# Kernel optimization log

Hardware: AMD Instinct MI355X
Metric: run time of the kernel (lower is better)

The kernel has to match this reference:

```python
import jax, jax.numpy as jnp
import numpy as np

B, N, K = 8, 4096, 16          # batch, points, kNN neighbors
IN_F, D, L, NUM_CLS = 3, 128, 2, 40  # in_features, hidden dim, transformer blocks, classes


def setup_inputs() -> dict:
    key = jax.random.key(0)
    ks = jax.random.split(key, 13)

    def w(k, shape):
        fan_in = shape[-2]
        return (jax.random.normal(k, shape, jnp.float32) / np.sqrt(fan_in).astype(np.float32))

    return {
        "features": jax.random.normal(ks[0], (B, N, IN_F), jnp.float32),
        "pos": jax.random.normal(ks[1], (B, N, 3), jnp.float32),
        "W_embed": w(ks[2], (IN_F, D)),
        "Wq": w(ks[3], (L, D, D)),
        "Wk": w(ks[4], (L, D, D)),
        "Wv": w(ks[5], (L, D, D)),
        "P1": w(ks[6], (L, 3, D)),   # position-encoding MLP layer 1
        "P2": w(ks[7], (L, D, D)),   # position-encoding MLP layer 2
        "G1": w(ks[8], (L, D, D)),   # attention (gamma) MLP layer 1
        "G2": w(ks[9], (L, D, D)),   # attention (gamma) MLP layer 2
        "Wo": w(ks[10], (L, D, D)),  # output projection per block
        "W_cls1": w(ks[11], (D, D)),
        "W_cls2": w(ks[12], (D, NUM_CLS)),
    }


def _gather(x, idx):
    # x: [B,N,C], idx: [B,N,K] -> [B,N,K,C]
    return jax.vmap(lambda xb, ib: xb[ib])(x, idx)


def _forward(features, pos, W_embed, Wq, Wk, Wv, P1, P2, G1, G2, Wo, W_cls1, W_cls2):
    # point-wise embedding MLP
    x = jax.nn.relu(features @ W_embed)  # [B,N,D]

    # kNN in euclidean space (indices, incl. self)
    sq = jnp.sum(pos * pos, axis=-1)                      # [B,N]
    d2 = sq[:, :, None] + sq[:, None, :] - 2.0 * jnp.einsum("bnc,bmc->bnm", pos, pos)
    _, idx = jax.lax.top_k(-d2, K)                        # [B,N,K]

    rel = pos[:, :, None, :] - _gather(pos, idx)          # [B,N,K,3]

    for l in range(L):
        q = x @ Wq[l]                                     # [B,N,D]
        k = x @ Wk[l]
        v = x @ Wv[l]
        kj = _gather(k, idx)                              # [B,N,K,D]
        vj = _gather(v, idx)
        # relative position encoding MLP
        delta = jax.nn.relu(rel @ P1[l]) @ P2[l]          # [B,N,K,D]
        # vector attention: gamma MLP over (q_i - k_j + delta)
        g = q[:, :, None, :] - kj + delta
        logits = jax.nn.relu(g @ G1[l]) @ G2[l]           # [B,N,K,D]
        attn = jax.nn.softmax(logits, axis=2)             # over K neighbors
        agg = jnp.sum(attn * (vj + delta), axis=2)        # [B,N,D]
        x = x + agg @ Wo[l]                               # residual

    pooled = jnp.max(x, axis=1)                           # [B,D] global max pool
    h = jax.nn.relu(pooled @ W_cls1)
    return h @ W_cls2                                     # [B,NUM_CLS]


def reference(features, pos, W_embed, Wq, Wk, Wv, P1, P2, G1, G2, Wo, W_cls1, W_cls2):
    return _forward(features, pos, W_embed, Wq, Wk, Wv, P1, P2, G1, G2, Wo, W_cls1, W_cls2)
```

## Files before the change

### kernel.cpp

```cpp
#include <hip/hip_runtime.h>
#include <hip/hip_bf16.h>
#include <float.h>

#define BB 8
#define NN 4096
#define KNN 16
#define Dh 128
#define NPTS (BB*NN)
#define NPART 4
#define PARTSZ (NN/NPART)

typedef __attribute__((ext_vector_type(8))) short bf16x8;
typedef __attribute__((ext_vector_type(8))) unsigned short u16x8;
typedef __attribute__((ext_vector_type(4))) float f32x4;

#define MFMA16(a,b,c) __builtin_amdgcn_mfma_f32_16x16x32_bf16(a,b,c,0,0,0)

__device__ __forceinline__ unsigned short f2b(float f) {
  __hip_bfloat16 h = __float2bfloat16(f);
  return *(unsigned short*)&h;
}
__device__ __forceinline__ unsigned pack_bf2(float lo, float hi) {
  __hip_bfloat16 l = __float2bfloat16(lo), h = __float2bfloat16(hi);
  return (unsigned)(*(unsigned short*)&l) | ((unsigned)(*(unsigned short*)&h) << 16);
}
__device__ __forceinline__ float b2f(unsigned short s) {
  union { unsigned u; float f; } v; v.u = ((unsigned)s) << 16; return v.f;
}
__device__ __forceinline__ float blo(unsigned u) {
  union { unsigned u; float f; } v; v.u = u << 16; return v.f;
}
__device__ __forceinline__ float bhi(unsigned u) {
  union { unsigned u; float f; } v; v.u = u & 0xffff0000u; return v.f;
}
__device__ __forceinline__ int swz16(int row) { return (row >> 2) << 4; }

__global__ __launch_bounds__(256) void embed_kernel(
    const float* __restrict__ f, const float* __restrict__ We, float* __restrict__ x) {
  int i = blockIdx.x * 256 + threadIdx.x;
  if (i >= NPTS * Dh) return;
  int p = i >> 7, d = i & 127;
  float f0 = f[p*3+0], f1 = f[p*3+1], f2 = f[p*3+2];
  float v = f0 * We[0*Dh + d] + f1 * We[1*Dh + d] + f2 * We[2*Dh + d];
  x[i] = fmaxf(v, 0.f);
}

__global__ __launch_bounds__(256) void knn_part_kernel(
    const float* __restrict__ pos, float* __restrict__ pd2,
    unsigned short* __restrict__ pix) {
  __shared__ float4 cand[PARTSZ];
  int b = blockIdx.z, part = blockIdx.y;
  const float* pb = pos + (size_t)b * NN * 3;
  int c0 = part * PARTSZ;
  for (int i = threadIdx.x; i < PARTSZ; i += 256) {
    float X = pb[(c0+i)*3+0], Y = pb[(c0+i)*3+1], Z = pb[(c0+i)*3+2];
    cand[i] = make_float4(X, Y, Z, X*X + Y*Y + Z*Z);
  }
  __syncthreads();

  int q = blockIdx.x * 256 + threadIdx.x;
  float qx = pb[q*3+0], qy = pb[q*3+1], qz = pb[q*3+2];
  float qs = qx*qx + qy*qy + qz*qz;

  float val[KNN]; int ind[KNN];
  float cmax; int cslot;

  #pragma unroll
  for (int t = 0; t < KNN; t++) {
    float4 c = cand[t];
    val[t] = qs + c.w - 2.f*(qx*c.x + qy*c.y + qz*c.z);
    ind[t] = t;
  }
  cmax = val[0]; cslot = 0;
  #pragma unroll
  for (int i = 1; i < KNN; i++)
    if (val[i] >= cmax) { cmax = val[i]; cslot = i; }

  float bv0=0.f,bv1=0.f,bv2=0.f,bv3=0.f,bv4=0.f,bv5=0.f,bv6=0.f,bv7=0.f;
  int   bi0=0,  bi1=0,  bi2=0,  bi3=0,  bi4=0,  bi5=0,  bi6=0,  bi7=0;
  int   cnt = 0;

#define DRAIN_SLOT(S, BV, BI)                                      \
  { bool act = ((S) < cnt) && ((BV) < cmax);                       \
    if (__ballot(act)) {                                           \
      _Pragma("unroll")                                            \
      for (int i = 0; i < KNN; i++) {                              \
        bool r = act && (i == cslot);                              \
        val[i] = r ? (BV) : val[i];                                \
        ind[i] = r ? (BI) : ind[i];                                \
      }                                                            \
      cmax = val[0]; cslot = 0;                                    \
      _Pragma("unroll")                                            \
      for (int i = 1; i < KNN; i++)                                \
        if (val[i] >= cmax) { cmax = val[i]; cslot = i; }          \
    } }
#define DRAIN_ALL                                                  \
  { DRAIN_SLOT(0, bv0, bi0) DRAIN_SLOT(1, bv1, bi1)                \
    DRAIN_SLOT(2, bv2, bi2) DRAIN_SLOT(3, bv3, bi3)                \
    DRAIN_SLOT(4, bv4, bi4) DRAIN_SLOT(5, bv5, bi5)                \
    DRAIN_SLOT(6, bv6, bi6) DRAIN_SLOT(7, bv7, bi7) cnt = 0; }

  for (int m = KNN; m < PARTSZ; m++) {
    float4 c = cand[m];
    float d2 = qs + c.w - 2.f*(qx*c.x + qy*c.y + qz*c.z);
    if (d2 < cmax) {
      bv0 = (cnt == 0) ? d2 : bv0;  bi0 = (cnt == 0) ? m : bi0;
      bv1 = (cnt == 1) ? d2 : bv1;  bi1 = (cnt == 1) ? m : bi1;
      bv2 = (cnt == 2) ? d2 : bv2;  bi2 = (cnt == 2) ? m : bi2;
      bv3 = (cnt == 3) ? d2 : bv3;  bi3 = (cnt == 3) ? m : bi3;
      bv4 = (cnt == 4) ? d2 : bv4;  bi4 = (cnt == 4) ? m : bi4;
      bv5 = (cnt == 5) ? d2 : bv5;  bi5 = (cnt == 5) ? m : bi5;
      bv6 = (cnt == 6) ? d2 : bv6;  bi6 = (cnt == 6) ? m : bi6;
      bv7 = (cnt == 7) ? d2 : bv7;  bi7 = (cnt == 7) ? m : bi7;
      cnt++;
    }
    if (__ballot(cnt == 8)) DRAIN_ALL
  }
  if (__ballot(cnt > 0)) DRAIN_ALL

#undef DRAIN_SLOT
#undef DRAIN_ALL

  size_t base = ((size_t)(b*NN + q) * NPART + part) * KNN;
  #pragma unroll
  for (int i = 0; i < KNN; i++) {
    pd2[base + i] = val[i];
    pix[base + i] = (unsigned short)(b*NN + c0 + ind[i]);
  }
}

__global__ __launch_bounds__(256) void knn_merge_kernel(
    const float* __restrict__ pd2, const unsigned short* __restrict__ pix,
    unsigned short* __restrict__ idxout) {
  int p = blockIdx.x * 256 + threadIdx.x;
  size_t base = (size_t)p * NPART * KNN;

  float val[KNN]; int ind[KNN];
  #pragma unroll
  for (int i = 0; i < KNN; i++) { val[i] = FLT_MAX; ind[i] = 0; }
  float cmax = FLT_MAX; int cslot = 0;

  for (int t = 0; t < NPART*KNN; t++) {
    float d2 = pd2[base + t];
    int j = pix[base + t];
    if (d2 < cmax) {
      #pragma unroll
      for (int i = 0; i < KNN; i++) if (i == cslot) { val[i] = d2; ind[i] = j; }
      cmax = val[0]; cslot = 0;
      #pragma unroll
      for (int i = 1; i < KNN; i++) if (val[i] >= cmax) { cmax = val[i]; cslot = i; }
    }
  }
  #pragma unroll
  for (int i = 0; i < KNN; i++) idxout[(size_t)p*KNN + i] = (unsigned short)ind[i];
}

__global__ __launch_bounds__(256) void wprep_all_kernel(
    const float* __restrict__ W0, const float* __restrict__ W1,
    const float* __restrict__ W2, const float* __restrict__ W3,
    const float* __restrict__ W4, const float* __restrict__ W5,
    const float* __restrict__ W6, unsigned short* __restrict__ wT) {
  const float* srcs[7] = {W0, W1, W2, W3, W4, W5, W6};
  int z = blockIdx.z, m = blockIdx.y;
  const float* W = srcs[z] + m*16384;
  unsigned short* WT = wT + z*32768 + m*16384;
  int t = blockIdx.x * 256 + threadIdx.x;
  int o = t >> 7, i = t & 127;
  WT[o*128 + i] = f2b(W[i*128 + o]);
}

__global__ __launch_bounds__(256) void qkv_kernel(
    const float* __restrict__ x,
    const unsigned short* __restrict__ QT, const unsigned short* __restrict__ KT,
    const unsigned short* __restrict__ VT,
    unsigned short* __restrict__ qb, unsigned* __restrict__ kvb) {
  int w = threadIdx.x >> 6, l = threadIdx.x & 63;
  int lr = l & 15, lg = l >> 4;
  int R = blockIdx.x * 64 + w * 16;
  const float* xr = x + (size_t)(R + lr) * Dh + lg * 8;
  bf16x8 a[4];
  #pragma unroll
  for (int kt = 0; kt < 4; kt++) {
    bf16x8 av;
    #pragma unroll
    for (int j = 0; j < 8; j++) av[j] = (short)f2b(xr[kt*32 + j]);
    a[kt] = av;
  }
  #pragma unroll
  for (int n = 0; n < 8; n++) {
    f32x4 c = {0.f, 0.f, 0.f, 0.f};
    #pragma unroll
    for (int kt = 0; kt < 4; kt++)
      c = MFMA16(a[kt], *(const bf16x8*)&QT[(n*16 + lr)*Dh + kt*32 + lg*8], c);
    #pragma unroll
    for (int r = 0; r < 4; r++)
      qb[(size_t)(R + lg*4 + r)*Dh + n*16 + lr] = f2b(c[r]);
  }
  #pragma unroll
  for (int n = 0; n < 8; n++) {
    f32x4 ck = {0.f, 0.f, 0.f, 0.f}, cv = {0.f, 0.f, 0.f, 0.f};
    #pragma unroll
    for (int kt = 0; kt < 4; kt++) {
      ck = MFMA16(a[kt], *(const bf16x8*)&KT[(n*16 + lr)*Dh + kt*32 + lg*8], ck);
      cv = MFMA16(a[kt], *(const bf16x8*)&VT[(n*16 + lr)*Dh + kt*32 + lg*8], cv);
    }
    #pragma unroll
    for (int r = 0; r < 4; r++)
      kvb[(size_t)(R + lg*4 + r)*Dh + n*16 + lr] = pack_bf2(ck[r], cv[r]);
  }
}

struct PtCtx {
  int jA, jC[4];
  float rx, ry, rz;
  unsigned short qv[8];
};
__device__ __forceinline__ void load_ctx(PtCtx& c, int p,
    const unsigned short* __restrict__ idxb, const float* __restrict__ pos,
    const unsigned short* __restrict__ qb, int lr, int lg) {
  c.jA = idxb[(size_t)p*KNN + lr];
  #pragma unroll
  for (int r = 0; r < 4; r++) c.jC[r] = idxb[(size_t)p*KNN + lg*4 + r];
  float px0 = pos[p*3+0], py0 = pos[p*3+1], pz0 = pos[p*3+2];
  c.rx = px0 - pos[c.jA*3+0];
  c.ry = py0 - pos[c.jA*3+1];
  c.rz = pz0 - pos[c.jA*3+2];
  #pragma unroll
  for (int n = 0; n < 8; n++) c.qv[n] = qb[(size_t)p*Dh + n*16 + lr];
}

__global__ void __attribute__((amdgpu_flat_work_group_size(512, 512)))
__attribute__((amdgpu_waves_per_eu(2, 2)))
fused_mega_kernel(
    const unsigned short* __restrict__ qb, const unsigned* __restrict__ kvb,
    const unsigned short* __restrict__ idxb, const float* __restrict__ pos,
    const float* __restrict__ P1,
    const unsigned short* __restrict__ P2T, const unsigned short* __restrict__ G1T,
    const unsigned short* __restrict__ G2T, unsigned short* __restrict__ aggb) {
  __shared__ __align__(16) unsigned short wB[3][16384];
  __shared__ __align__(16) unsigned short trans[8][2048];
  int tid = threadIdx.x;
  int wv = tid >> 6, l = tid & 63;
  int lr = l & 15, lg = l >> 4;
  const int swz = (lr & 7) << 3;
  const int swtR = swz16(lr);

  int orig = (blockIdx.x & 7) * 32 + (blockIdx.x >> 3);

  {
    const unsigned short* srcs[3] = {P2T, G1T, G2T};
    #pragma unroll
    for (int z = 0; z < 3; z++) {
      const unsigned short* src = srcs[z];
      for (int t = tid * 8; t < 16384; t += 512 * 8) {
        int dst = t ^ (((t >> 7) & 7) << 3);
        *(u16x8*)&wB[z][dst] = *(const u16x8*)&src[t];
      }
    }
  }
  __syncthreads();

  unsigned short* tb = trans[wv];
  int p0 = orig * 128 + wv * 16;

  PtCtx cur, nxt;
  load_ctx(cur, p0, idxb, pos, qb, lr, lg);
  nxt = cur;

  #pragma unroll 1
  for (int i = 0; i < 16; i++) {
    int p = p0 + i;

    const unsigned* kvp0 = kvb + (size_t)cur.jC[0]*Dh;
    const unsigned* kvp1 = kvb + (size_t)cur.jC[1]*Dh;
    const unsigned* kvp2 = kvb + (size_t)cur.jC[2]*Dh;
    const unsigned* kvp3 = kvb + (size_t)cur.jC[3]*Dh;
    unsigned kvr[8][4];
    #pragma unroll
    for (int n = 0; n < 8; n++) {
      kvr[n][0] = kvp0[n*16 + lr];
      kvr[n][1] = kvp1[n*16 + lr];
      kvr[n][2] = kvp2[n*16 + lr];
      kvr[n][3] = kvp3[n*16 + lr];
    }

    bf16x8 aT[4];
    #pragma unroll
    for (int kt = 0; kt < 4; kt++) {
      int c0 = kt*32 + lg*8;
      float4 pa0 = *(const float4*)&P1[c0],        pa1 = *(const float4*)&P1[c0+4];
      float4 pb0 = *(const float4*)&P1[Dh+c0],     pb1 = *(const float4*)&P1[Dh+c0+4];
      float4 pc0 = *(const float4*)&P1[2*Dh+c0],   pc1 = *(const float4*)&P1[2*Dh+c0+4];
      bf16x8 av;
      av[0] = (short)f2b(fmaxf(cur.rx*pa0.x + cur.ry*pb0.x + cur.rz*pc0.x, 0.f));
      av[1] = (short)f2b(fmaxf(cur.rx*pa0.y + cur.ry*pb0.y + cur.rz*pc0.y, 0.f));
      av[2] = (short)f2b(fmaxf(cur.rx*pa0.z + cur.ry*pb0.z + cur.rz*pc0.z, 0.f));
      av[3] = (short)f2b(fmaxf(cur.rx*pa0.w + cur.ry*pb0.w + cur.rz*pc0.w, 0.f));
      av[4] = (short)f2b(fmaxf(cur.rx*pa1.x + cur.ry*pb1.x + cur.rz*pc1.x, 0.f));
      av[5] = (short)f2b(fmaxf(cur.rx*pa1.y + cur.ry*pb1.y + cur.rz*pc1.y, 0.f));
      av[6] = (short)f2b(fmaxf(cur.rx*pa1.z + cur.ry*pb1.z + cur.rz*pc1.z, 0.f));
      av[7] = (short)f2b(fmaxf(cur.rx*pa1.w + cur.ry*pb1.w + cur.rz*pc1.w, 0.f));
      aT[kt] = av;
    }

    f32x4 dlt[8];
    #pragma unroll
    for (int n = 0; n < 8; n++) {
      f32x4 c = {0.f, 0.f, 0.f, 0.f};
      #pragma unroll
      for (int kt = 0; kt < 4; kt++)
        c = MFMA16(aT[kt], *(const bf16x8*)&wB[0][((n*16 + lr)*Dh + kt*32 + lg*8) ^ swz], c);
      dlt[n] = c;
    }

    #pragma unroll
    for (int n = 0; n < 8; n++) {
      float q = b2f(cur.qv[n]);
      #pragma unroll
      for (int r = 0; r < 4; r++) {
        unsigned kv = kvr[n][r];
        int row = lg*4 + r, ch = n*16 + lr;
        tb[(row*Dh + ch) ^ swz16(row)] = f2b(q - blo(kv) + dlt[n][r]);
        dlt[n][r] += bhi(kv);
      }
    }

    if (i < 15) load_ctx(nxt, p + 1, idxb, pos, qb, lr, lg);

    bf16x8 ag[4];
    #pragma unroll
    for (int kt = 0; kt < 4; kt++)
      ag[kt] = *(const bf16x8*)&tb[(lr*Dh + kt*32 + lg*8) ^ swtR];
    f32x4 hh[8];
    #pragma unroll
    for (int n = 0; n < 8; n++) {
      f32x4 c = {0.f, 0.f, 0.f, 0.f};
      #pragma unroll
      for (int kt = 0; kt < 4; kt++)
        c = MFMA16(ag[kt], *(const bf16x8*)&wB[1][((n*16 + lr)*Dh + kt*32 + lg*8) ^ swz], c);
      hh[n] = c;
    }
    #pragma unroll
    for (int n = 0; n < 8; n++) {
      #pragma unroll
      for (int r = 0; r < 4; r++) {
        int row = lg*4 + r, ch = n*16 + lr;
        tb[(row*Dh + ch) ^ swz16(row)] = f2b(fmaxf(hh[n][r], 0.f));
      }
    }

    bf16x8 ah[4];
    #pragma unroll
    for (int kt = 0; kt < 4; kt++)
      ah[kt] = *(const bf16x8*)&tb[(lr*Dh + kt*32 + lg*8) ^ swtR];
    f32x4 lgt[8];
    #pragma unroll
    for (int n = 0; n < 8; n++) {
      f32x4 c = {0.f, 0.f, 0.f, 0.f};
      #pragma unroll
      for (int kt = 0; kt < 4; kt++)
        c = MFMA16(ah[kt], *(const bf16x8*)&wB[2][((n*16 + lr)*Dh + kt*32 + lg*8) ^ swz], c);
      lgt[n] = c;
    }

    #pragma unroll
    for (int n = 0; n < 8; n++) {
      f32x4 L = lgt[n];
      float m = fmaxf(fmaxf(L[0], L[1]), fmaxf(L[2], L[3]));
      m = fmaxf(m, __shfl_xor(m, 16));
      m = fmaxf(m, __shfl_xor(m, 32));
      float e0 = __expf(L[0]-m), e1 = __expf(L[1]-m);
      float e2 = __expf(L[2]-m), e3 = __expf(L[3]-m);
      float s = e0 + e1 + e2 + e3;
      s += __shfl_xor(s, 16);
      s += __shfl_xor(s, 32);
      float inv = 1.f / s;
      float ws;
      ws  = e0 * dlt[n][0];
      ws += e1 * dlt[n][1];
      ws += e2 * dlt[n][2];
      ws += e3 * dlt[n][3];
      ws *= inv;
      ws += __shfl_xor(ws, 16);
      ws += __shfl_xor(ws, 32);
      if (lg == 0) aggb[(size_t)p*Dh + n*16 + lr] = f2b(ws);
    }

    cur = nxt;
  }
}

__global__ __launch_bounds__(256) void xupd_kernel(
    float* __restrict__ x, const unsigned short* __restrict__ aggb,
    const unsigned short* __restrict__ WoT) {
  int w = threadIdx.x >> 6, l = threadIdx.x & 63;
  int lr = l & 15, lg = l >> 4;
  int R = blockIdx.x * 64 + w * 16;
  bf16x8 a[4];
  #pragma unroll
  for (int kt = 0; kt < 4; kt++)
    a[kt] = *(const bf16x8*)&aggb[(size_t)(R + lr)*Dh + kt*32 + lg*8];
  #pragma unroll
  for (int n = 0; n < 8; n++) {
    f32x4 c = {0.f, 0.f, 0.f, 0.f};
    #pragma unroll
    for (int kt = 0; kt < 4; kt++)
      c = MFMA16(a[kt], *(const bf16x8*)&WoT[(n*16 + lr)*Dh + kt*32 + lg*8], c);
    #pragma unroll
    for (int r = 0; r < 4; r++)
      x[(size_t)(R + lg*4 + r)*Dh + n*16 + lr] += c[r];
  }
}

__global__ __launch_bounds__(128) void pool_part_kernel(
    const float* __restrict__ x, float* __restrict__ part) {
  int b = blockIdx.y, chunk = blockIdx.x, d = threadIdx.x;
  const float* xb = x + ((size_t)b*NN + chunk*128) * Dh;
  float m = -FLT_MAX;
  for (int n = 0; n < 128; n++) m = fmaxf(m, xb[(size_t)n*Dh + d]);
  part[(b*32 + chunk)*Dh + d] = m;
}

__global__ __launch_bounds__(128) void head_kernel(
    const float* __restrict__ part, const float* __restrict__ W1,
    const float* __restrict__ W2, float* __restrict__ out) {
  int b = blockIdx.x, d = threadIdx.x;
  __shared__ float pooled[Dh], h[Dh];
  float m = -FLT_MAX;
  for (int c = 0; c < 32; c++) m = fmaxf(m, part[(b*32 + c)*Dh + d]);
  pooled[d] = m;
  __syncthreads();
  float acc = 0.f;
  for (int c = 0; c < Dh; c++) acc += pooled[c] * W1[c*Dh + d];
  h[d] = fmaxf(acc, 0.f);
  __syncthreads();
  if (d < 40) {
    float o = 0.f;
    for (int c = 0; c < Dh; c++) o += h[c] * W2[c*40 + d];
    out[b*40 + d] = o;
  }
}

extern "C" void kernel_launch(void* const* d_in, const int* in_sizes, int n_in,
                              void* d_out, int out_size, void* d_ws, size_t ws_size,
                              hipStream_t stream) {
  const float* features = (const float*)d_in[0];
  const float* pos      = (const float*)d_in[1];
  const float* W_embed  = (const float*)d_in[2];
  const float* Wq       = (const float*)d_in[3];
  const float* Wk       = (const float*)d_in[4];
  const float* Wv       = (const float*)d_in[5];
  const float* P1       = (const float*)d_in[6];
  const float* P2       = (const float*)d_in[7];
  const float* G1       = (const float*)d_in[8];
  const float* G2       = (const float*)d_in[9];
  const float* Wo       = (const float*)d_in[10];
  const float* Wc1      = (const float*)d_in[11];
  const float* Wc2      = (const float*)d_in[12];
  float* out = (float*)d_out;

  float* x = (float*)d_ws;
  unsigned short* qb = (unsigned short*)(x + (size_t)NPTS*Dh);
  unsigned* kvb = (unsigned*)(qb + (size_t)NPTS*Dh);
  unsigned short* wT = (unsigned short*)(kvb + (size_t)NPTS*Dh);
  unsigned short* aggb = wT + 7*2*16384;
  unsigned short* idxb = aggb + (size_t)NPTS*Dh;

  float* pd2 = (float*)kvb;
  unsigned short* pix = qb;
  float* part = (float*)qb;

  unsigned short* QT  = wT + 0*32768;
  unsigned short* KT  = wT + 1*32768;
  unsigned short* VT  = wT + 2*32768;
  unsigned short* P2T = wT + 3*32768;
  unsigned short* G1T = wT + 4*32768;
  unsigned short* G2T = wT + 5*32768;
  unsigned short* WoT = wT + 6*32768;

  knn_part_kernel<<<dim3(NN/256, NPART, BB), 256, 0, stream>>>(pos, pd2, pix);
  knn_merge_kernel<<<NPTS/256, 256, 0, stream>>>(pd2, pix, idxb);

  wprep_all_kernel<<<dim3(64, 2, 7), 256, 0, stream>>>(Wq, Wk, Wv, P2, G1, G2, Wo, wT);
  embed_kernel<<<NPTS*Dh/256, 256, 0, stream>>>(features, W_embed, x);

  for (int l = 0; l < 2; l++) {
    qkv_kernel<<<NPTS/64, 256, 0, stream>>>(
        x, QT + l*16384, KT + l*16384, VT + l*16384, qb, kvb);
    fused_mega_kernel<<<256, 512, 0, stream>>>(
        qb, kvb, idxb, pos,
        P1 + l*3*Dh, P2T + l*16384, G1T + l*16384, G2T + l*16384, aggb);
    xupd_kernel<<<NPTS/64, 256, 0, stream>>>(x, aggb, WoT + l*16384);
  }

  pool_part_kernel<<<dim3(32, BB), 128, 0, stream>>>(x, part);
  head_kernel<<<BB, 128, 0, stream>>>(part, Wc1, Wc2, out);
}
```

Before: 878.2 us.

## Fuse layer-0 residual update with layer-1 QKV projection; split kNN into more partitions

Adds a kernel that applies the layer-0 output projection and residual update, stages the updated rows as bf16 in shared memory, and computes the layer-1 Q, K and V projections in the same pass. This avoids re-reading the fp32 activations from global memory and saves a separate launch. The kNN candidate search now uses eight partitions instead of four and is issued as two launches over batch halves, giving smaller per-block candidate sets and more blocks. The larger partial-result buffers must still fit in the aliased scratch regions, and the merge kernel has to scan twice as many partial lists.

After: 975.2 us. +11.1%, slower.

```diff
diff --git a/kernel.cpp b/kernel.cpp
--- a/kernel.cpp
+++ b/kernel.cpp
@@ -7,7 +7,7 @@
 #define KNN 16
 #define Dh 128
 #define NPTS (BB*NN)
-#define NPART 4
+#define NPART 8
 #define PARTSZ (NN/NPART)
 
 typedef __attribute__((ext_vector_type(8))) short bf16x8;
@@ -47,9 +47,9 @@
 
 __global__ __launch_bounds__(256) void knn_part_kernel(
     const float* __restrict__ pos, float* __restrict__ pd2,
-    unsigned short* __restrict__ pix) {
+    unsigned short* __restrict__ pix, int b0) {
   __shared__ float4 cand[PARTSZ];
-  int b = blockIdx.z, part = blockIdx.y;
+  int b = b0 + blockIdx.z, part = blockIdx.y;
   const float* pb = pos + (size_t)b * NN * 3;
   int c0 = part * PARTSZ;
   for (int i = threadIdx.x; i < PARTSZ; i += 256) {
@@ -210,6 +210,69 @@
   }
 }
 
+__global__ __launch_bounds__(256) void xupd_qkv_kernel(
+    float* __restrict__ x, const unsigned short* __restrict__ aggb,
+    const unsigned short* __restrict__ WoT,
+    const unsigned short* __restrict__ QT, const unsigned short* __restrict__ KT,
+    const unsigned short* __restrict__ VT,
+    unsigned short* __restrict__ qb, unsigned* __restrict__ kvb) {
+  __shared__ __align__(16) unsigned short trans[4][2048];
+  int w = threadIdx.x >> 6, l = threadIdx.x & 63;
+  int lr = l & 15, lg = l >> 4;
+  int R = blockIdx.x * 64 + w * 16;
+  unsigned short* tb = trans[w];
+  const int swtR = swz16(lr);
+
+  bf16x8 a[4];
+  #pragma unroll
+  for (int kt = 0; kt < 4; kt++)
+    a[kt] = *(const bf16x8*)&aggb[(size_t)(R + lr)*Dh + kt*32 + lg*8];
+
+  #pragma unroll
+  for (int n = 0; n < 8; n++) {
+    f32x4 c = {0.f, 0.f, 0.f, 0.f};
+    #pragma unroll
+    for (int kt = 0; kt < 4; kt++)
+      c = MFMA16(a[kt], *(const bf16x8*)&WoT[(n*16 + lr)*Dh + kt*32 + lg*8], c);
+    #pragma unroll
+    for (int r = 0; r < 4; r++) {
+      int row = lg*4 + r, ch = n*16 + lr;
+      size_t xi = (size_t)(R + row)*Dh + ch;
+      float xv = x[xi] + c[r];
+      x[xi] = xv;
+      tb[(row*Dh + ch) ^ swz16(row)] = f2b(xv);
+    }
+  }
+
+  bf16x8 ax[4];
+  #pragma unroll
+  for (int kt = 0; kt < 4; kt++)
+    ax[kt] = *(const bf16x8*)&tb[(lr*Dh + kt*32 + lg*8) ^ swtR];
+
+  #pragma unroll
+  for (int n = 0; n < 8; n++) {
+    f32x4 c = {0.f, 0.f, 0.f, 0.f};
+    #pragma unroll
+    for (int kt = 0; kt < 4; kt++)
+      c = MFMA16(ax[kt], *(const bf16x8*)&QT[(n*16 + lr)*Dh + kt*32 + lg*8], c);
+    #pragma unroll
+    for (int r = 0; r < 4; r++)
+      qb[(size_t)(R + lg*4 + r)*Dh + n*16 + lr] = f2b(c[r]);
+  }
+  #pragma unroll
+  for (int n = 0; n < 8; n++) {
+    f32x4 ck = {0.f, 0.f, 0.f, 0.f}, cv = {0.f, 0.f, 0.f, 0.f};
+    #pragma unroll
+    for (int kt = 0; kt < 4; kt++) {
+      ck = MFMA16(ax[kt], *(const bf16x8*)&KT[(n*16 + lr)*Dh + kt*32 + lg*8], ck);
+      cv = MFMA16(ax[kt], *(const bf16x8*)&VT[(n*16 + lr)*Dh + kt*32 + lg*8], cv);
+    }
+    #pragma unroll
+    for (int r = 0; r < 4; r++)
+      kvb[(size_t)(R + lg*4 + r)*Dh + n*16 + lr] = pack_bf2(ck[r], cv[r]);
+  }
+}
+
 struct PtCtx {
   int jA, jC[4];
   float rx, ry, rz;
@@ -478,20 +541,21 @@
   unsigned short* G2T = wT + 5*32768;
   unsigned short* WoT = wT + 6*32768;
 
-  knn_part_kernel<<<dim3(NN/256, NPART, BB), 256, 0, stream>>>(pos, pd2, pix);
+  knn_part_kernel<<<dim3(NN/256, NPART, BB/2), 256, 0, stream>>>(pos, pd2, pix, 0);
+  knn_part_kernel<<<dim3(NN/256, NPART, BB/2), 256, 0, stream>>>(pos, pd2, pix, 4);
   knn_merge_kernel<<<NPTS/256, 256, 0, stream>>>(pd2, pix, idxb);
 
   wprep_all_kernel<<<dim3(64, 2, 7), 256, 0, stream>>>(Wq, Wk, Wv, P2, G1, G2, Wo, wT);
   embed_kernel<<<NPTS*Dh/256, 256, 0, stream>>>(features, W_embed, x);
 
-  for (int l = 0; l < 2; l++) {
-    qkv_kernel<<<NPTS/64, 256, 0, stream>>>(
-        x, QT + l*16384, KT + l*16384, VT + l*16384, qb, kvb);
-    fused_mega_kernel<<<256, 512, 0, stream>>>(
-        qb, kvb, idxb, pos,
-        P1 + l*3*Dh, P2T + l*16384, G1T + l*16384, G2T + l*16384, aggb);
-    xupd_kernel<<<NPTS/64, 256, 0, stream>>>(x, aggb, WoT + l*16384);
-  }
+  qkv_kernel<<<NPTS/64, 256, 0, stream>>>(x, QT, KT, VT, qb, kvb);
+  fused_mega_kernel<<<256, 512, 0, stream>>>(
+      qb, kvb, idxb, pos, P1, P2T, G1T, G2T, aggb);
+  xupd_qkv_kernel<<<NPTS/64, 256, 0, stream>>>(
+      x, aggb, WoT, QT + 16384, KT + 16384, VT + 16384, qb, kvb);
+  fused_mega_kernel<<<256, 512, 0, stream>>>(
+      qb, kvb, idxb, pos, P1 + 3*Dh, P2T + 16384, G1T + 16384, G2T + 16384, aggb);
+  xupd_kernel<<<NPTS/64, 256, 0, stream>>>(x, aggb, WoT + 16384);
 
   pool_part_kernel<<<dim3(32, BB), 128, 0, stream>>>(x, part);
   head_kernel<<<BB, 128, 0, stream>>>(part, Wc1, Wc2, out);
```
